# Kernel optimization log

Hardware: AMD Instinct MI355X
Metric: run time of the kernel (lower is better)

## Reference

```python
import jax, jax.numpy as jnp
import numpy as np

LORA_DIM = 16          # hard-coded in module
LORA_TOKEN_INDEX = 1   # lora_dim*layer_sequence + 1 with layer_sequence=0
B, S, D, H = 4, 2048, 1024, 4096  # num_hiddens = 4*num_input (forced by view())


def setup_inputs() -> dict:
    key = jax.random.key(0)
    ks = jax.random.split(key, 6)
    x = jax.random.normal(ks[0], (B, S, D), dtype=jnp.float32)
    W1 = jax.random.normal(ks[1], (H, D), dtype=jnp.float32) * 0.02
    b1 = jnp.zeros((H,), dtype=jnp.float32)
    W2 = jax.random.normal(ks[2], (D, H), dtype=jnp.float32) * 0.02
    b2 = jnp.zeros((D,), dtype=jnp.float32)
    scale = jnp.asarray(0.001, dtype=jnp.float32)  # nn.Parameter(torch.tensor(0.001))
    return {"x": x, "W1": W1, "b1": b1, "W2": W2, "b2": b2, "scale": scale}


def reference(x, W1, b1, W2, b2, scale):
    Bx, Sx, Dx = x.shape
    Hx = W1.shape[0]  # = 4*Dx
    # 16 lora tokens starting at LORA_TOKEN_INDEX
    lt = jax.lax.dynamic_slice_in_dim(x, LORA_TOKEN_INDEX, LORA_DIM, axis=1)
    even = lt[:, ::2, :]  # (B, 8, D)
    odd = lt[:, 1::2, :]  # (B, 8, D)
    # per-sample low-rank weight updates:
    # result_multiplication[b,k] = outer(even[b,k], odd[b,k]) (D,D)
    # matrix1 = first 4 blocks stacked -> (B, 4D, D); matrix2 = last 4 reshaped -> (B, D, 4D)
    m1 = (even[:, :4, :, None] * odd[:, :4, None, :]).reshape(Bx, Hx, Dx)
    m2 = (even[:, 4:, :, None] * odd[:, 4:, None, :]).reshape(Bx, Dx, Hx)
    # x @ (W1 + scale*m1)^T + b1, fused without repeating W1 per batch
    h = jnp.einsum('bsd,hd->bsh', x, W1) + scale * jnp.einsum('bsd,bhd->bsh', x, m1) + b1
    h = jax.nn.gelu(h, approximate=False)  # torch nn.GELU default = exact erf
    out = jnp.einsum('bsh,oh->bso', h, W2) + scale * jnp.einsum('bsh,boh->bso', h, m2) + b2
    return out
```

## Files before the change

kernel.cpp:

```cpp
#include <hip/hip_runtime.h>
#include <cstdint>
#include <cstddef>

#define MROWS 8192
#define DDIM  1024
#define HDIM  4096

typedef __bf16 bf16x8 __attribute__((ext_vector_type(8)));
typedef float  f32x4  __attribute__((ext_vector_type(4)));

typedef __attribute__((address_space(1))) void* as1_vp;
typedef __attribute__((address_space(3))) void* as3_vp;

__device__ __forceinline__ unsigned short f2bf(float f) {
  unsigned int u = __builtin_bit_cast(unsigned int, f);
  u += 0x7fffu + ((u >> 16) & 1u);
  return (unsigned short)(u >> 16);
}
__device__ __forceinline__ float bf2f(unsigned short h) {
  return __builtin_bit_cast(float, (unsigned int)h << 16);
}

__device__ __forceinline__ float fast_gelu(float x) {
  float x3 = x * x * x;
  float z = 0.7978845608028654f * x + 0.03567740814f * x3;
  float e = __builtin_amdgcn_exp2f(z * 2.8853900817779268f);
  float t = 1.0f - 2.0f * __builtin_amdgcn_rcpf(e + 1.0f);
  return 0.5f * x * (1.0f + t);
}

__device__ __forceinline__ void gld_lds16(const unsigned short* g, unsigned short* lds) {
  __builtin_amdgcn_global_load_lds((as1_vp)(uintptr_t)g, (as3_vp)lds, 16, 0, 0);
}

__global__ __launch_bounds__(256) void pre_kernel(
    const float* __restrict__ x, const float* __restrict__ w1,
    const float* __restrict__ w2, unsigned short* __restrict__ xb,
    unsigned short* __restrict__ w1b, unsigned short* __restrict__ w2b,
    float* __restrict__ p1) {
  if (blockIdx.x < 8192) {
    int i = blockIdx.x * 256 + threadIdx.x;
    const float* src; unsigned short* dst; int off;
    if (i < 1048576) { src = w1; dst = w1b; off = i; }
    else             { src = w2; dst = w2b; off = i - 1048576; }
    float4 v = ((const float4*)src)[off];
    ushort4 o;
    o.x = f2bf(v.x); o.y = f2bf(v.y); o.z = f2bf(v.z); o.w = f2bf(v.w);
    ((ushort4*)dst)[off] = o;
    return;
  }
  const int bid = blockIdx.x - 8192;
  const int wave = threadIdx.x >> 6, lane = threadIdx.x & 63;
  const int m = bid * 4 + wave;
  const int b = m >> 11;
  const float4* xrow4 = (const float4*)(x + (size_t)m * DDIM);
  const float4* od4   = (const float4*)(x + ((size_t)b * 2048 + 2) * DDIM);
  ushort4* xbrow4 = (ushort4*)(xb + (size_t)m * DDIM);
  float a0 = 0.f, a1 = 0.f, a2 = 0.f, a3 = 0.f;
#pragma unroll
  for (int it = 0; it < 4; ++it) {
    int g = it * 64 + lane;
    float4 v = xrow4[g];
    ushort4 o; o.x = f2bf(v.x); o.y = f2bf(v.y); o.z = f2bf(v.z); o.w = f2bf(v.w);
    xbrow4[g] = o;
    float4 o0 = od4[g];
    float4 o1 = od4[512 + g];
    float4 o2 = od4[1024 + g];
    float4 o3 = od4[1536 + g];
    a0 += v.x * o0.x + v.y * o0.y + v.z * o0.z + v.w * o0.w;
    a1 += v.x * o1.x + v.y * o1.y + v.z * o1.z + v.w * o1.w;
    a2 += v.x * o2.x + v.y * o2.y + v.z * o2.z + v.w * o2.w;
    a3 += v.x * o3.x + v.y * o3.y + v.z * o3.z + v.w * o3.w;
  }
#pragma unroll
  for (int off = 32; off > 0; off >>= 1) {
    a0 += __shfl_down(a0, off);
    a1 += __shfl_down(a1, off);
    a2 += __shfl_down(a2, off);
    a3 += __shfl_down(a3, off);
  }
  if (lane == 0) {
    float4 r; r.x = a0; r.y = a1; r.z = a2; r.w = a3;
    ((float4*)p1)[m] = r;
  }
}

__device__ __forceinline__ void gemm_bt_tile64(const unsigned short* __restrict__ A,
                                               const unsigned short* __restrict__ B,
                                               const int ld, const int Kloop,
                                               const int m0, const int n0,
                                               unsigned short* As, unsigned short* Bs,
                                               f32x4 acc[4][4]) {
  const int tid  = threadIdx.x;
  const int wave = tid >> 6;
  const int lane = tid & 63;
  const int quad = lane >> 4;
  const int l16  = lane & 15;
  const int wm   = (wave >> 1) * 64;
  const int wn   = (wave & 1) * 64;

  const unsigned short* ga[4]; const unsigned short* gb[4];
#pragma unroll
  for (int s = 0; s < 4; ++s) {
    int idx = wave * 256 + s * 64 + lane;
    int r = idx >> 3, sl = idx & 7;
    int c = (sl - r) & 7;
    ga[s] = A + (size_t)(m0 + r) * ld + c * 8;
    gb[s] = B + (size_t)(n0 + r) * ld + c * 8;
  }

  for (int k0 = 0; k0 < Kloop; k0 += 64) {
    __syncthreads();
#pragma unroll
    for (int s = 0; s < 4; ++s) gld_lds16(ga[s] + k0, As + (wave * 4 + s) * 512);
#pragma unroll
    for (int s = 0; s < 4; ++s) gld_lds16(gb[s] + k0, Bs + (wave * 4 + s) * 512);
    __syncthreads();
#pragma unroll
    for (int kk = 0; kk < 64; kk += 32) {
      bf16x8 a[4], b[4];
      const int cbase = (kk >> 3) + quad;
#pragma unroll
      for (int i = 0; i < 4; ++i) {
        const int ra = wm + i * 16 + l16;
        const int rb = wn + i * 16 + l16;
        a[i] = *(const bf16x8*)(As + ra * 64 + ((cbase + ra) & 7) * 8);
        b[i] = *(const bf16x8*)(Bs + rb * 64 + ((cbase + rb) & 7) * 8);
      }
#pragma unroll
      for (int i = 0; i < 4; ++i)
#pragma unroll
        for (int j = 0; j < 4; ++j)
          acc[i][j] = __builtin_amdgcn_mfma_f32_16x16x32_bf16(a[i], b[j], acc[i][j], 0, 0, 0);
    }
  }
}

__global__ __launch_bounds__(256) void gemm1_kernel(
    const unsigned short* __restrict__ xb, const unsigned short* __restrict__ w1b,
    const float* __restrict__ x, const float* __restrict__ b1,
    const float* __restrict__ p1, const float* __restrict__ scale_p,
    unsigned short* __restrict__ hact) {
  __shared__ __align__(16) unsigned short As[128 * 64];
  __shared__ __align__(16) unsigned short Bs[128 * 64];
  const int id = blockIdx.x;
  const int xcd = id & 7, w = id >> 3;
  const int m0 = (xcd * 8 + (w & 7)) * 128;
  const int n0 = (w >> 3) * 128;
  f32x4 acc[4][4];
  const f32x4 z = {0.f, 0.f, 0.f, 0.f};
#pragma unroll
  for (int i = 0; i < 4; ++i)
#pragma unroll
    for (int j = 0; j < 4; ++j) acc[i][j] = z;

  gemm_bt_tile64(xb, w1b, DDIM, DDIM, m0, n0, As, Bs, acc);

  const int tid = threadIdx.x;
  const int wave = tid >> 6, lane = tid & 63, quad = lane >> 4, l16 = lane & 15;
  const int wm = (wave >> 1) * 64, wn = (wave & 1) * 64;
  const float sc = scale_p[0];
  const int bidx = m0 >> 11;
  const int i1 = (n0 + wn) >> 10;
  const float* exrow = x + ((size_t)(bidx * 2048 + 1 + 2 * i1)) * DDIM;

  float exv[4], b1v[4]; int nn[4];
#pragma unroll
  for (int j = 0; j < 4; ++j) {
    nn[j]  = n0 + wn + j * 16 + l16;
    exv[j] = exrow[nn[j] & 1023];
    b1v[j] = b1[nn[j]];
  }
#pragma unroll
  for (int i = 0; i < 4; ++i) {
#pragma unroll
    for (int r = 0; r < 4; ++r) {
      const int m = m0 + wm + i * 16 + quad * 4 + r;
      const float pv = p1[(size_t)m * 4 + i1] * sc;
#pragma unroll
      for (int j = 0; j < 4; ++j) {
        float v = acc[i][j][r] + b1v[j] + pv * exv[j];
        hact[(size_t)m * HDIM + nn[j]] = f2bf(fast_gelu(v));
      }
    }
  }
}

__global__ __launch_bounds__(256) void gemm2_kernel(
    const unsigned short* __restrict__ hact, const unsigned short* __restrict__ w2b,
    const float* __restrict__ x, const float* __restrict__ b2,
    const float* __restrict__ scale_p, float* __restrict__ out) {
  __shared__ __align__(16) unsigned short As[128 * 128];
  __shared__ __align__(16) unsigned short Bs[128 * 128];
  __shared__ __align__(16) unsigned short od_lds[1024];
  __shared__ __align__(16) float p2s[128 * 4];
  const int id = blockIdx.x;
  const int xcd = id & 7, w = id >> 3;
  const int m0 = (xcd * 8 + (w >> 3)) * 128;
  const int n0 = (w & 7) * 128;
  const int tid = threadIdx.x;
  const int wave = tid >> 6, lane = tid & 63, quad = lane >> 4, l16 = lane & 15;
  const int wm = (wave >> 1) * 64, wn = (wave & 1) * 64;
  const int bidx = m0 >> 11;
  const int i2 = n0 >> 8;

  {
    const float4* src = (const float4*)(x + ((size_t)(bidx * 2048 + 10 + 2 * i2)) * DDIM);
    float4 v = src[tid];
    ushort4 o; o.x = f2bf(v.x); o.y = f2bf(v.y); o.z = f2bf(v.z); o.w = f2bf(v.w);
    ((ushort4*)od_lds)[tid] = o;
  }

  f32x4 acc[4][4];
  const f32x4 z = {0.f, 0.f, 0.f, 0.f};
#pragma unroll
  for (int i = 0; i < 4; ++i)
#pragma unroll
    for (int j = 0; j < 4; ++j) acc[i][j] = z;
  f32x4 pacc[4] = {z, z, z, z};
  const bf16x8 zer8 = __builtin_bit_cast(bf16x8, z);

  const unsigned short* ga[8]; const unsigned short* gb[8];
#pragma unroll
  for (int s = 0; s < 8; ++s) {
    int idx = wave * 512 + s * 64 + lane;
    int r = idx >> 4, sl = idx & 15;
    int c = (sl - r) & 15;
    ga[s] = hact + (size_t)(m0 + r) * HDIM + c * 8;
    gb[s] = w2b  + (size_t)(n0 + r) * HDIM + c * 8;
  }

  for (int k0 = 0; k0 < HDIM; k0 += 128) {
    __syncthreads();
#pragma unroll
    for (int s = 0; s < 8; ++s) gld_lds16(ga[s] + k0, As + (wave * 8 + s) * 512);
#pragma unroll
    for (int s = 0; s < 8; ++s) gld_lds16(gb[s] + k0, Bs + (wave * 8 + s) * 512);
    __syncthreads();
    const int odbase = k0 & 1023;
#pragma unroll
    for (int kk = 0; kk < 128; kk += 32) {
      bf16x8 a[4], b[4];
      const int cbase = (kk >> 3) + quad;
#pragma unroll
      for (int i = 0; i < 4; ++i) {
        const int ra = wm + i * 16 + l16;
        const int rb = wn + i * 16 + l16;
        a[i] = *(const bf16x8*)(As + ra * 128 + ((cbase + ra) & 15) * 8);
        b[i] = *(const bf16x8*)(Bs + rb * 128 + ((cbase + rb) & 15) * 8);
      }
      if (wn == 0) {
        bf16x8 odv = *(const bf16x8*)(od_lds + odbase + kk + quad * 8);
        bf16x8 bod = (l16 == 0) ? odv : zer8;
#pragma unroll
        for (int i = 0; i < 4; ++i)
          pacc[i] = __builtin_amdgcn_mfma_f32_16x16x32_bf16(a[i], bod, pacc[i], 0, 0, 0);
      }
#pragma unroll
      for (int i = 0; i < 4; ++i)
#pragma unroll
        for (int j = 0; j < 4; ++j)
          acc[i][j] = __builtin_amdgcn_mfma_f32_16x16x32_bf16(a[i], b[j], acc[i][j], 0, 0, 0);
    }
    if (((k0 + 128) & 1023) == 0) {
      const int seg = k0 >> 10;
      if (wn == 0) {
        if (l16 == 0) {
#pragma unroll
          for (int i = 0; i < 4; ++i)
#pragma unroll
            for (int e = 0; e < 4; ++e)
              p2s[(wm + i * 16 + quad * 4 + e) * 4 + seg] = pacc[i][e];
        }
#pragma unroll
        for (int i = 0; i < 4; ++i) pacc[i] = z;
      }
    }
  }
  __syncthreads();

  const float sc = scale_p[0];
  const float* evrow = x + ((size_t)(bidx * 2048 + 9 + 2 * i2)) * DDIM;

  float4 ev[4]; float b2v[4]; int nn[4];
#pragma unroll
  for (int j = 0; j < 4; ++j) {
    nn[j] = n0 + wn + j * 16 + l16;
    ev[j]  = *(const float4*)(evrow + 4 * (nn[j] & 255));
    b2v[j] = b2[nn[j]];
  }
#pragma unroll
  for (int i = 0; i < 4; ++i) {
#pragma unroll
    for (int r = 0; r < 4; ++r) {
      const int mloc = wm + i * 16 + quad * 4 + r;
      const int m = m0 + mloc;
      const float4 pv = *(const float4*)(p2s + mloc * 4);
#pragma unroll
      for (int j = 0; j < 4; ++j) {
        float lora = ev[j].x * pv.x + ev[j].y * pv.y + ev[j].z * pv.z + ev[j].w * pv.w;
        out[(size_t)m * DDIM + nn[j]] = acc[i][j][r] + b2v[j] + sc * lora;
      }
    }
  }
}

extern "C" void kernel_launch(void* const* d_in, const int* in_sizes, int n_in,
                              void* d_out, int out_size, void* d_ws, size_t ws_size,
                              hipStream_t stream) {
  const float* x     = (const float*)d_in[0];
  const float* W1    = (const float*)d_in[1];
  const float* b1    = (const float*)d_in[2];
  const float* W2    = (const float*)d_in[3];
  const float* b2    = (const float*)d_in[4];
  const float* scale = (const float*)d_in[5];
  float* out = (float*)d_out;

  char* ws = (char*)d_ws;
  unsigned short* xb   = (unsigned short*)(ws);
  unsigned short* w1b  = (unsigned short*)(ws + 16777216);
  unsigned short* w2b  = (unsigned short*)(ws + 25165824);
  unsigned short* hact = (unsigned short*)(ws + 33554432);
  float*          p1   = (float*)(ws + 100663296);

  pre_kernel<<<dim3(10240), dim3(256), 0, stream>>>(x, W1, W2, xb, w1b, w2b, p1);
  gemm1_kernel<<<dim3(2048), dim3(256), 0, stream>>>(xb, w1b, x, b1, p1, scale, hact);
  gemm2_kernel<<<dim3(512), dim3(256), 0, stream>>>(hact, w2b, x, b2, scale, out);
}
```

Before: 277.1 us.

## Rewrite gemm1 with 256x256 tiles, 512 threads and 4-stage LDS pipeline

```diff
diff --git a/kernel.cpp b/kernel.cpp
--- a/kernel.cpp
+++ b/kernel.cpp
@@ -85,97 +85,124 @@
   }
 }
 
-__device__ __forceinline__ void gemm_bt_tile64(const unsigned short* __restrict__ A,
-                                               const unsigned short* __restrict__ B,
-                                               const int ld, const int Kloop,
-                                               const int m0, const int n0,
-                                               unsigned short* As, unsigned short* Bs,
-                                               f32x4 acc[4][4]) {
-  const int tid  = threadIdx.x;
-  const int wave = tid >> 6;
-  const int lane = tid & 63;
-  const int quad = lane >> 4;
-  const int l16  = lane & 15;
-  const int wm   = (wave >> 1) * 64;
-  const int wn   = (wave & 1) * 64;
-
-  const unsigned short* ga[4]; const unsigned short* gb[4];
-#pragma unroll
-  for (int s = 0; s < 4; ++s) {
-    int idx = wave * 256 + s * 64 + lane;
-    int r = idx >> 3, sl = idx & 7;
-    int c = (sl - r) & 7;
-    ga[s] = A + (size_t)(m0 + r) * ld + c * 8;
-    gb[s] = B + (size_t)(n0 + r) * ld + c * 8;
-  }
-
-  for (int k0 = 0; k0 < Kloop; k0 += 64) {
-    __syncthreads();
-#pragma unroll
-    for (int s = 0; s < 4; ++s) gld_lds16(ga[s] + k0, As + (wave * 4 + s) * 512);
-#pragma unroll
-    for (int s = 0; s < 4; ++s) gld_lds16(gb[s] + k0, Bs + (wave * 4 + s) * 512);
-    __syncthreads();
-#pragma unroll
-    for (int kk = 0; kk < 64; kk += 32) {
-      bf16x8 a[4], b[4];
-      const int cbase = (kk >> 3) + quad;
-#pragma unroll
-      for (int i = 0; i < 4; ++i) {
-        const int ra = wm + i * 16 + l16;
-        const int rb = wn + i * 16 + l16;
-        a[i] = *(const bf16x8*)(As + ra * 64 + ((cbase + ra) & 7) * 8);
-        b[i] = *(const bf16x8*)(Bs + rb * 64 + ((cbase + rb) & 7) * 8);
-      }
-#pragma unroll
-      for (int i = 0; i < 4; ++i)
-#pragma unroll
-        for (int j = 0; j < 4; ++j)
-          acc[i][j] = __builtin_amdgcn_mfma_f32_16x16x32_bf16(a[i], b[j], acc[i][j], 0, 0, 0);
-    }
-  }
-}
-
-__global__ __launch_bounds__(256) void gemm1_kernel(
+#define VMW(n) asm volatile("s_waitcnt vmcnt(" #n ")" ::: "memory")
+#define LKW()  asm volatile("s_waitcnt lgkmcnt(0)" ::: "memory")
+#define BAR()  asm volatile("s_barrier" ::: "memory")
+
+__global__ __launch_bounds__(512, 2) void gemm1_kernel(
     const unsigned short* __restrict__ xb, const unsigned short* __restrict__ w1b,
     const float* __restrict__ x, const float* __restrict__ b1,
     const float* __restrict__ p1, const float* __restrict__ scale_p,
     unsigned short* __restrict__ hact) {
-  __shared__ __align__(16) unsigned short As[128 * 64];
-  __shared__ __align__(16) unsigned short Bs[128 * 64];
+  __shared__ __align__(16) unsigned short As[4 * 256 * 32];
+  __shared__ __align__(16) unsigned short Bs[4 * 256 * 32];
+
   const int id = blockIdx.x;
   const int xcd = id & 7, w = id >> 3;
-  const int m0 = (xcd * 8 + (w & 7)) * 128;
-  const int n0 = (w >> 3) * 128;
-  f32x4 acc[4][4];
+  const int m0 = (xcd * 4 + (w & 3)) * 256;
+  const int n0 = (w >> 2) * 256;
+
+  const int tid  = threadIdx.x;
+  const int wave = tid >> 6, lane = tid & 63;
+  const int quad = lane >> 4, l16 = lane & 15;
+  const int wm2  = wave >> 2;
+  const int wn2  = wave & 3;
+
+  const unsigned short *gA0, *gA1, *gB0, *gB1;
+  {
+    int idx = tid;
+    int r = idx >> 2, sl = idx & 3, c = (sl - (r >> 1)) & 3;
+    gA0 = xb  + (size_t)(m0 + r) * DDIM + c * 8;
+    gB0 = w1b + (size_t)(n0 + r) * DDIM + c * 8;
+    idx = 512 + tid;
+    r = idx >> 2; sl = idx & 3; c = (sl - (r >> 1)) & 3;
+    gA1 = xb  + (size_t)(m0 + r) * DDIM + c * 8;
+    gB1 = w1b + (size_t)(n0 + r) * DDIM + c * 8;
+  }
+  const int ldsOff0 = (wave * 64) * 8;
+  const int ldsOff1 = (512 + wave * 64) * 8;
+
+#define STAGE1(tt, sb) do {                                   \
+    const int _k = (tt) * 32;                                 \
+    unsigned short* _a = &As[(sb) * 8192];                    \
+    unsigned short* _b = &Bs[(sb) * 8192];                    \
+    gld_lds16(gA0 + _k, _a + ldsOff0);                        \
+    gld_lds16(gA1 + _k, _a + ldsOff1);                        \
+    gld_lds16(gB0 + _k, _b + ldsOff0);                        \
+    gld_lds16(gB1 + _k, _b + ldsOff1);                        \
+  } while (0)
+
+  f32x4 acc[8][4];
   const f32x4 z = {0.f, 0.f, 0.f, 0.f};
 #pragma unroll
-  for (int i = 0; i < 4; ++i)
+  for (int i = 0; i < 8; ++i)
 #pragma unroll
     for (int j = 0; j < 4; ++j) acc[i][j] = z;
 
-  gemm_bt_tile64(xb, w1b, DDIM, DDIM, m0, n0, As, Bs, acc);
-
-  const int tid = threadIdx.x;
-  const int wave = tid >> 6, lane = tid & 63, quad = lane >> 4, l16 = lane & 15;
-  const int wm = (wave >> 1) * 64, wn = (wave & 1) * 64;
+  auto compute_tile = [&](const unsigned short* __restrict__ Ab,
+                          const unsigned short* __restrict__ Bb) {
+    bf16x8 a[8], b[4];
+#pragma unroll
+    for (int j = 0; j < 4; ++j) {
+      const int rb = wn2 * 64 + j * 16 + l16;
+      b[j] = *(const bf16x8*)(Bb + rb * 32 + ((quad + (rb >> 1)) & 3) * 8);
+    }
+#pragma unroll
+    for (int i = 0; i < 8; ++i) {
+      const int ra = wm2 * 128 + i * 16 + l16;
+      a[i] = *(const bf16x8*)(Ab + ra * 32 + ((quad + (ra >> 1)) & 3) * 8);
+    }
+    __builtin_amdgcn_s_setprio(1);
+#pragma unroll
+    for (int i = 0; i < 8; ++i)
+#pragma unroll
+      for (int j = 0; j < 4; ++j)
+        acc[i][j] = __builtin_amdgcn_mfma_f32_16x16x32_bf16(a[i], b[j], acc[i][j], 0, 0, 0);
+    __builtin_amdgcn_s_setprio(0);
+  };
+
+#define TILE_FULL(tt, cb, sb) do {                            \
+    STAGE1((tt) + 3, sb);                                     \
+    VMW(12);                                                  \
+    BAR();                                                    \
+    compute_tile(&As[(cb) * 8192], &Bs[(cb) * 8192]);         \
+    LKW();                                                    \
+    BAR();                                                    \
+  } while (0)
+
+  STAGE1(0, 0);
+  STAGE1(1, 1);
+  STAGE1(2, 2);
+
+#pragma unroll 1
+  for (int t = 0; t < 28; t += 4) {
+    TILE_FULL(t + 0, 0, 3);
+    TILE_FULL(t + 1, 1, 0);
+    TILE_FULL(t + 2, 2, 1);
+    TILE_FULL(t + 3, 3, 2);
+  }
+  TILE_FULL(28, 0, 3);
+  VMW(8);  BAR(); compute_tile(&As[1 * 8192], &Bs[1 * 8192]);
+  VMW(4);  BAR(); compute_tile(&As[2 * 8192], &Bs[2 * 8192]);
+  VMW(0);  BAR(); compute_tile(&As[3 * 8192], &Bs[3 * 8192]);
+
   const float sc = scale_p[0];
   const int bidx = m0 >> 11;
-  const int i1 = (n0 + wn) >> 10;
+  const int i1 = (n0 + wn2 * 64) >> 10;
   const float* exrow = x + ((size_t)(bidx * 2048 + 1 + 2 * i1)) * DDIM;
 
   float exv[4], b1v[4]; int nn[4];
 #pragma unroll
   for (int j = 0; j < 4; ++j) {
-    nn[j]  = n0 + wn + j * 16 + l16;
+    nn[j]  = n0 + wn2 * 64 + j * 16 + l16;
     exv[j] = exrow[nn[j] & 1023];
     b1v[j] = b1[nn[j]];
   }
 #pragma unroll
-  for (int i = 0; i < 4; ++i) {
+  for (int i = 0; i < 8; ++i) {
 #pragma unroll
     for (int r = 0; r < 4; ++r) {
-      const int m = m0 + wm + i * 16 + quad * 4 + r;
+      const int m = m0 + wm2 * 128 + i * 16 + quad * 4 + r;
       const float pv = p1[(size_t)m * 4 + i1] * sc;
 #pragma unroll
       for (int j = 0; j < 4; ++j) {
@@ -184,6 +211,8 @@
       }
     }
   }
+#undef TILE_FULL
+#undef STAGE1
 }
 
 __global__ __launch_bounds__(256) void gemm2_kernel(
@@ -324,6 +353,6 @@
   float*          p1   = (float*)(ws + 100663296);
 
   pre_kernel<<<dim3(10240), dim3(256), 0, stream>>>(x, W1, W2, xb, w1b, w2b, p1);
-  gemm1_kernel<<<dim3(2048), dim3(256), 0, stream>>>(xb, w1b, x, b1, p1, scale, hact);
+  gemm1_kernel<<<dim3(512), dim3(512), 0, stream>>>(xb, w1b, x, b1, p1, scale, hact);
   gemm2_kernel<<<dim3(512), dim3(256), 0, stream>>>(hact, w2b, x, b2, scale, out);
 }
```

Measured after the change: 266.4 us. 1.04x faster.
